# Optimization experiments

Hardware: AMD Instinct MI355X
Metric: run time of the kernel (lower is better)

The kernel has to match this reference:

```python
import jax, jax.numpy as jnp
import numpy as np

DIM = 1024
H = 16
HD = DIM // H  # 64
SCALE = HD ** -0.5
EPS = 1e-5


def setup_inputs() -> dict:
    key = jax.random.key(0)
    ks = jax.random.split(key, 8)
    B, N = 2, 2048
    x = jax.random.normal(ks[0], (B, N, DIM), dtype=jnp.float32)
    qkv_w = jax.random.normal(ks[1], (5 * DIM, DIM), dtype=jnp.float32) * (DIM ** -0.5)
    proj_w = jax.random.normal(ks[2], (DIM, DIM), dtype=jnp.float32) * (DIM ** -0.5)
    proj_b = jnp.zeros((DIM,), dtype=jnp.float32)
    lambda_q1 = jax.random.normal(ks[3], (HD,), dtype=jnp.float32) * 0.1
    lambda_k1 = jax.random.normal(ks[4], (HD,), dtype=jnp.float32) * 0.1
    lambda_q2 = jax.random.normal(ks[5], (HD,), dtype=jnp.float32) * 0.1
    lambda_k2 = jax.random.normal(ks[6], (HD,), dtype=jnp.float32) * 0.1
    return {"x": x, "qkv_w": qkv_w, "proj_w": proj_w, "proj_b": proj_b,
            "lambda_q1": lambda_q1, "lambda_k1": lambda_k1,
            "lambda_q2": lambda_q2, "lambda_k2": lambda_k2}


def reference(x, qkv_w, proj_w, proj_b, lambda_q1, lambda_k1, lambda_q2, lambda_k2):
    B, N, C = x.shape
    # qkv projection -> (5, B, H, N, hd)
    qkv = jnp.einsum('bnc,fc->bnf', x, qkv_w).reshape(B, N, 5, H, HD)
    qkv = jnp.transpose(qkv, (2, 0, 3, 1, 4))
    q1, q2, k1, k2, v = qkv[0], qkv[1], qkv[2], qkv[3], qkv[4]
    # dual attention score matrices (B, H, N, N)
    attn1 = jax.nn.softmax(jnp.einsum('bhqd,bhkd->bhqk', q1, k1) * SCALE, axis=-1)
    attn2 = jax.nn.softmax(jnp.einsum('bhqd,bhkd->bhqk', q2, k2) * SCALE, axis=-1)
    lambda_full = (jnp.exp(jnp.sum(lambda_q1 * lambda_k1))
                   - jnp.exp(jnp.sum(lambda_q2 * lambda_k2)) + 0.8)
    attn = attn1 - lambda_full * attn2
    out = jnp.einsum('bhqk,bhkd->bhqd', attn, v)  # (B,H,N,hd)
    out = jnp.transpose(out, (0, 2, 1, 3)).reshape(B, N, C)
    # RMSNorm (no affine) over last dim, then fixed scale (1 - 0.8)
    out = out * jax.lax.rsqrt(jnp.mean(out * out, axis=-1, keepdims=True) + EPS)
    out = out * (1.0 - 0.8)
    return jnp.einsum('bnc,oc->bno', out, proj_w) + proj_b
```

## Files before the change

### kernel.cpp

```cpp
#include <hip/hip_runtime.h>
#include <hip/hip_bf16.h>

#define SEQ   2048
#define BATCH 2
#define NHEAD 16
#define HDIM  64
#define CDIM  1024
#define QKV_F 5120
#define SCALE 0.125f
#define LOG2E 1.44269504f
#define EPSV  1e-5f

typedef __bf16 bf16;
typedef __bf16 bf16x4 __attribute__((ext_vector_type(4)));
typedef __bf16 bf16x8 __attribute__((ext_vector_type(8)));
typedef float  f32x4  __attribute__((ext_vector_type(4)));

#define MFMA16(a, b, c) __builtin_amdgcn_mfma_f32_16x16x32_bf16(a, b, c, 0, 0, 0)

__device__ __forceinline__ unsigned pkbf(float a, float b) {
    union { bf16 h[2]; unsigned u; } t;
    t.h[0] = (bf16)a; t.h[1] = (bf16)b;
    return t.u;
}
__device__ __forceinline__ unsigned short bfbits(float a) {
    union { bf16 h; unsigned short u; } t;
    t.h = (bf16)a;
    return t.u;
}
__device__ __forceinline__ void gload16(const void* g, void* l) {
    __builtin_amdgcn_global_load_lds(
        (const __attribute__((address_space(1))) unsigned int*)g,
        (__attribute__((address_space(3))) unsigned int*)l, 16, 0, 0);
}

__global__ __launch_bounds__(256) void cvt_bf16(
    const float* __restrict__ s, bf16* __restrict__ d)
{
    const int i = (blockIdx.x * 256 + threadIdx.x) * 8;
    float4 a = *(const float4*)(s + i);
    float4 b = *(const float4*)(s + i + 4);
    bf16x8 t;
    t[0] = (bf16)a.x; t[1] = (bf16)a.y; t[2] = (bf16)a.z; t[3] = (bf16)a.w;
    t[4] = (bf16)b.x; t[5] = (bf16)b.y; t[6] = (bf16)b.z; t[7] = (bf16)b.w;
    *(bf16x8*)(d + i) = t;
}

template <int EPI>
__global__ __launch_bounds__(256) void gemm_lds(
    const bf16* __restrict__ A, const bf16* __restrict__ Bw,
    const float* __restrict__ bias,
    bf16* __restrict__ outq, float* __restrict__ outp,
    int M, int Nn, int K)
{
    __shared__ __align__(16) bf16 As[128 * 64];
    __shared__ __align__(16) bf16 Bs[128 * 64];

    const int tid  = threadIdx.x;
    const int lane = tid & 63;
    const int wave = tid >> 6;
    const int wr = wave >> 1, wc = wave & 1;
    const int g = lane >> 4, fr = lane & 15;
    const int m0 = blockIdx.y * 128;
    const int n0 = blockIdx.x * 128;

    const int lrow = lane >> 3;
    const int lcol = (lane & 7) << 3;

    f32x4 acc[4][4];
#pragma unroll
    for (int m = 0; m < 4; ++m)
#pragma unroll
        for (int n = 0; n < 4; ++n) acc[m][n] = f32x4{0.f, 0.f, 0.f, 0.f};

    const int nkt = K >> 6;
    for (int kt = 0; kt < nkt; ++kt) {
        const int k0 = kt << 6;
        __syncthreads();
#pragma unroll
        for (int i = 0; i < 4; ++i) {
            const int chunk = wave * 4 + i;
            const int row = chunk * 8 + lrow;
            gload16(A + (size_t)(m0 + row) * K + k0 + lcol, As + chunk * 512);
            gload16(Bw + (size_t)(n0 + row) * K + k0 + lcol, Bs + chunk * 512);
        }
        __syncthreads();
#pragma unroll
        for (int ks = 0; ks < 2; ++ks) {
            bf16x8 af[4], bfr[4];
#pragma unroll
            for (int m = 0; m < 4; ++m)
                af[m] = *(const bf16x8*)(As + (wr * 64 + m * 16 + fr) * 64 + ks * 32 + g * 8);
#pragma unroll
            for (int n = 0; n < 4; ++n)
                bfr[n] = *(const bf16x8*)(Bs + (wc * 64 + n * 16 + fr) * 64 + ks * 32 + g * 8);
#pragma unroll
            for (int m = 0; m < 4; ++m)
#pragma unroll
                for (int n = 0; n < 4; ++n)
                    acc[m][n] = MFMA16(af[m], bfr[n], acc[m][n]);
        }
    }

#pragma unroll
    for (int m = 0; m < 4; ++m) {
#pragma unroll
        for (int n = 0; n < 4; ++n) {
            const int row0 = m0 + wr * 64 + m * 16 + g * 4;
            const int col  = n0 + wc * 64 + n * 16 + fr;
            if (EPI == 0) {
                const int bb = row0 >> 11, nn = row0 & (SEQ - 1);
                const int sI = col >> 10, rem = col & (CDIM - 1);
                const int hh = rem >> 6, dd = rem & 63;
                const size_t base = ((size_t)((sI * BATCH + bb) * NHEAD + hh)) << 17;
                if (sI == 4) {
                    const int t4 = (nn >> 2) & 15;
                    const int G = t4 >> 3, jh = (t4 >> 2) & 1, gg = t4 & 3;
                    const int u = (G << 3) | (gg << 1) | jh;
                    const int nnp = (nn & ~63) | (u << 2);
                    ushort4 uu;
                    uu.x = bfbits(acc[m][n][0]);
                    uu.y = bfbits(acc[m][n][1]);
                    uu.z = bfbits(acc[m][n][2]);
                    uu.w = bfbits(acc[m][n][3]);
                    *(ushort4*)(outq + base + ((size_t)dd << 11) + nnp) = uu;
                } else {
                    const float sc = (sI < 2) ? SCALE * LOG2E : 1.f;
#pragma unroll
                    for (int r = 0; r < 4; ++r)
                        outq[base + ((size_t)(nn + r) << 6) + dd] = (bf16)(acc[m][n][r] * sc);
                }
            } else {
#pragma unroll
                for (int r = 0; r < 4; ++r)
                    outp[(size_t)(row0 + r) * Nn + col] = acc[m][n][r] + bias[col];
            }
        }
    }
}

__global__ __launch_bounds__(512, 2) void diff_attn(
    const bf16* __restrict__ qkv,
    const float* __restrict__ lq1, const float* __restrict__ lk1,
    const float* __restrict__ lq2, const float* __restrict__ lk2,
    float* __restrict__ attn_out)
{
    __shared__ __align__(16) char SM[49152];

    const int tid = threadIdx.x;
    const int lane = tid & 63, wave = tid >> 6;
    const int wg = wave & 3, grp = wave >> 2;
    const int g = lane >> 4, fr = lane & 15;
    const int bh = blockIdx.x, b = bh >> 4, h = bh & 15;
    const int q0 = blockIdx.y * 64 + wg * 16;
    const int kv0 = grp * (SEQ / 2);

    float ls1 = 0.f, ls2 = 0.f;
    for (int i = 0; i < HDIM; ++i) { ls1 += lq1[i] * lk1[i]; ls2 += lq2[i] * lk2[i]; }
    const float lam = __expf(ls1) - __expf(ls2) + 0.8f;

    const size_t HS = (size_t)SEQ * HDIM;
    const char* q1p = (const char*)(qkv + ((size_t)((0 * BATCH + b) * NHEAD + h)) * HS);
    const char* q2p = (const char*)(qkv + ((size_t)((1 * BATCH + b) * NHEAD + h)) * HS);
    const char* k1p = (const char*)(qkv + ((size_t)((2 * BATCH + b) * NHEAD + h)) * HS);
    const char* k2p = (const char*)(qkv + ((size_t)((3 * BATCH + b) * NHEAD + h)) * HS);
    const char* vtp = (const char*)(qkv + ((size_t)((4 * BATCH + b) * NHEAD + h)) * HS);

    bf16x8 qf1[2], qf2[2];
#pragma unroll
    for (int ks = 0; ks < 2; ++ks) {
        qf1[ks] = *(const bf16x8*)(q1p + (size_t)(q0 + fr) * 128 + ks * 64 + g * 16);
        qf2[ks] = *(const bf16x8*)(q2p + (size_t)(q0 + fr) * 128 + ks * 64 + g * 16);
    }

    const f32x4 z4{0.f, 0.f, 0.f, 0.f};
    f32x4 o1[4], o2[4];
#pragma unroll
    for (int d = 0; d < 4; ++d) { o1[d] = z4; o2[d] = z4; }
    f32x4 l1v = z4, l2v = z4;
    float m1 = -1e30f, m2 = -1e30f;

    const int lrow8 = lane >> 3;
    const int scol  = ((lane & 7) ^ lrow8) << 4;
    const int xw    = (fr & 7) << 4;

    char* base = SM + grp * 24576;
    const char* K1s = base;
    const char* K2s = base + 8192;
    const char* Vts = base + 16384;

    auto smax = [&](f32x4& s0, f32x4& s1, f32x4& s2, f32x4& s3,
                    float& mS, f32x4& lv, f32x4* o, unsigned* pw) {
        f32x4 t = __builtin_elementwise_max(
            __builtin_elementwise_max(s0, s1), __builtin_elementwise_max(s2, s3));
        float pm = fmaxf(fmaxf(t[0], t[1]), fmaxf(t[2], t[3]));
        pm = fmaxf(pm, __shfl_xor(pm, 16));
        pm = fmaxf(pm, __shfl_xor(pm, 32));
        if (!__all(pm <= mS + 8.f * LOG2E)) {
            float mn = fmaxf(mS, pm);
            float alpha = __builtin_amdgcn_exp2f(mS - mn);
            lv *= alpha;
#pragma unroll
            for (int d = 0; d < 4; ++d) o[d] *= alpha;
            mS = mn;
        }
#pragma unroll
        for (int r = 0; r < 4; ++r) {
            s0[r] = __builtin_amdgcn_exp2f(s0[r] - mS);
            s1[r] = __builtin_amdgcn_exp2f(s1[r] - mS);
            s2[r] = __builtin_amdgcn_exp2f(s2[r] - mS);
            s3[r] = __builtin_amdgcn_exp2f(s3[r] - mS);
        }
        lv += (s0 + s1) + (s2 + s3);
        pw[0] = pkbf(s0[0], s0[1]); pw[1] = pkbf(s0[2], s0[3]);
        pw[2] = pkbf(s1[0], s1[1]); pw[3] = pkbf(s1[2], s1[3]);
        pw[4] = pkbf(s2[0], s2[1]); pw[5] = pkbf(s2[2], s2[3]);
        pw[6] = pkbf(s3[0], s3[1]); pw[7] = pkbf(s3[2], s3[3]);
    };

#define KRD(Ks, n, ks) (*(const bf16x8*)((Ks) + ((n) * 16 + fr) * 128 + (((ks) * 64 + g * 16) ^ xw)))

    for (int kt = 0; kt < SEQ / 2 / 64; ++kt) {
        const int kvb = kv0 + kt * 64;
        __syncthreads();
#pragma unroll
        for (int i = 0; i < 6; ++i) {
            const int c = wg * 6 + i;
            const int t = c >> 3, ch = c & 7;
            const int row = ch * 8 + lrow8;
            char* ldst = base + t * 8192 + ch * 1024;
            const char* src;
            if (t == 0)      src = k1p + (size_t)(kvb + row) * 128 + scol;
            else if (t == 1) src = k2p + (size_t)(kvb + row) * 128 + scol;
            else             src = vtp + (size_t)row * (SEQ * 2) + (size_t)kvb * 2 + scol;
            gload16(src, ldst);
        }
        __syncthreads();

        f32x4 s10, s11, s12, s13;
        __builtin_amdgcn_s_setprio(1);
        s10 = MFMA16(KRD(K1s, 0, 0), qf1[0], z4);
        s11 = MFMA16(KRD(K1s, 1, 0), qf1[0], z4);
        s12 = MFMA16(KRD(K1s, 2, 0), qf1[0], z4);
        s13 = MFMA16(KRD(K1s, 3, 0), qf1[0], z4);
        s10 = MFMA16(KRD(K1s, 0, 1), qf1[1], s10);
        s11 = MFMA16(KRD(K1s, 1, 1), qf1[1], s11);
        s12 = MFMA16(KRD(K1s, 2, 1), qf1[1], s12);
        s13 = MFMA16(KRD(K1s, 3, 1), qf1[1], s13);
        __builtin_amdgcn_s_setprio(0);
        unsigned p1w[8];
        smax(s10, s11, s12, s13, m1, l1v, o1, p1w);

        f32x4 s20, s21, s22, s23;
        __builtin_amdgcn_s_setprio(1);
        s20 = MFMA16(KRD(K2s, 0, 0), qf2[0], z4);
        s21 = MFMA16(KRD(K2s, 1, 0), qf2[0], z4);
        s22 = MFMA16(KRD(K2s, 2, 0), qf2[0], z4);
        s23 = MFMA16(KRD(K2s, 3, 0), qf2[0], z4);
        s20 = MFMA16(KRD(K2s, 0, 1), qf2[1], s20);
        s21 = MFMA16(KRD(K2s, 1, 1), qf2[1], s21);
        s22 = MFMA16(KRD(K2s, 2, 1), qf2[1], s22);
        s23 = MFMA16(KRD(K2s, 3, 1), qf2[1], s23);
        __builtin_amdgcn_s_setprio(0);
        unsigned p2w[8];
        smax(s20, s21, s22, s23, m2, l2v, o2, p2w);

        __builtin_amdgcn_s_setprio(1);
#pragma unroll
        for (int G = 0; G < 2; ++G) {
            union { unsigned u[4]; bf16x8 v; } pf1, pf2;
#pragma unroll
            for (int w = 0; w < 4; ++w) { pf1.u[w] = p1w[G * 4 + w]; pf2.u[w] = p2w[G * 4 + w]; }
#pragma unroll
            for (int ds = 0; ds < 4; ++ds) {
                const int vrow = ds * 16 + fr;
                bf16x8 vf = *(const bf16x8*)(Vts + vrow * 128 +
                              ((G * 64 + g * 16) ^ ((vrow & 7) << 4)));
                o1[ds] = MFMA16(vf, pf1.v, o1[ds]);
                o2[ds] = MFMA16(vf, pf2.v, o2[ds]);
            }
        }
        __builtin_amdgcn_s_setprio(0);
    }
#undef KRD

    float l1 = (l1v[0] + l1v[1]) + (l1v[2] + l1v[3]);
    float l2 = (l2v[0] + l2v[1]) + (l2v[2] + l2v[3]);
    l1 += __shfl_xor(l1, 16); l1 += __shfl_xor(l1, 32);
    l2 += __shfl_xor(l2, 16); l2 += __shfl_xor(l2, 32);

    float* MF = (float*)SM;
    float* OF = (float*)(SM + 4096);
    __syncthreads();
    if (grp == 1) {
        const int p = tid - 256;
        MF[0 * 256 + p] = m1; MF[1 * 256 + p] = l1;
        MF[2 * 256 + p] = m2; MF[3 * 256 + p] = l2;
#pragma unroll
        for (int ds = 0; ds < 4; ++ds)
#pragma unroll
            for (int r = 0; r < 4; ++r) {
                OF[(ds * 4 + r) * 256 + p]        = o1[ds][r];
                OF[(16 + ds * 4 + r) * 256 + p]   = o2[ds][r];
            }
    }
    __syncthreads();
    if (grp == 0) {
        const float mB1 = MF[0 * 256 + tid], lB1 = MF[1 * 256 + tid];
        const float mB2 = MF[2 * 256 + tid], lB2 = MF[3 * 256 + tid];
        const float mn1 = fmaxf(m1, mB1), mn2 = fmaxf(m2, mB2);
        const float aA1 = __builtin_amdgcn_exp2f(m1 - mn1);
        const float aB1 = __builtin_amdgcn_exp2f(mB1 - mn1);
        const float aA2 = __builtin_amdgcn_exp2f(m2 - mn2);
        const float aB2 = __builtin_amdgcn_exp2f(mB2 - mn2);
        const float L1 = l1 * aA1 + lB1 * aB1;
        const float L2 = l2 * aA2 + lB2 * aB2;
        const float i1 = 1.f / L1;
        const float i2 = lam / L2;
        float* op = attn_out + ((size_t)(b * SEQ + q0 + fr)) * CDIM + h * HDIM;
#pragma unroll
        for (int ds = 0; ds < 4; ++ds) {
            float4 o;
#pragma unroll
            for (int r = 0; r < 4; ++r) {
                const float v1 = o1[ds][r] * aA1 + OF[(ds * 4 + r) * 256 + tid] * aB1;
                const float v2 = o2[ds][r] * aA2 + OF[(16 + ds * 4 + r) * 256 + tid] * aB2;
                ((float*)&o)[r] = v1 * i1 - i2 * v2;
            }
            *(float4*)(op + ds * 16 + g * 4) = o;
        }
    }
}

__global__ __launch_bounds__(256) void rmsnorm_bf16(
    const float* __restrict__ in, bf16* __restrict__ out)
{
    __shared__ float red[4];
    const int row = blockIdx.x, tid = threadIdx.x;
    const float4 v = ((const float4*)(in + (size_t)row * CDIM))[tid];
    float ss = v.x * v.x + v.y * v.y + v.z * v.z + v.w * v.w;
#pragma unroll
    for (int m = 1; m < 64; m <<= 1) ss += __shfl_xor(ss, m);
    if ((tid & 63) == 0) red[tid >> 6] = ss;
    __syncthreads();
    float tot = red[0] + red[1] + red[2] + red[3];
    float sc = rsqrtf(tot * (1.f / CDIM) + EPSV) * 0.2f;
    bf16x4 o;
    o[0] = (bf16)(v.x * sc); o[1] = (bf16)(v.y * sc);
    o[2] = (bf16)(v.z * sc); o[3] = (bf16)(v.w * sc);
    ((bf16x4*)(out + (size_t)row * CDIM))[tid] = o;
}

extern "C" void kernel_launch(void* const* d_in, const int* in_sizes, int n_in,
                              void* d_out, int out_size, void* d_ws, size_t ws_size,
                              hipStream_t stream)
{
    (void)in_sizes; (void)n_in; (void)out_size; (void)ws_size;
    const float* x      = (const float*)d_in[0];
    const float* qkv_w  = (const float*)d_in[1];
    const float* proj_w = (const float*)d_in[2];
    const float* proj_b = (const float*)d_in[3];
    const float* lq1    = (const float*)d_in[4];
    const float* lk1    = (const float*)d_in[5];
    const float* lq2    = (const float*)d_in[6];
    const float* lk2    = (const float*)d_in[7];
    float* out = (float*)d_out;

    char* ws = (char*)d_ws;
    bf16*  qkv_t    = (bf16*)ws;
    bf16*  attn_b   = (bf16*)ws;
    float* attn_out = (float*)(ws + (size_t)40 * 1024 * 1024);
    bf16*  x_b      = (bf16*)(ws + (size_t)40 * 1024 * 1024);
    bf16*  qkvw_b   = (bf16*)(ws + (size_t)56 * 1024 * 1024);
    bf16*  projw_b  = (bf16*)(ws + (size_t)66 * 1024 * 1024);

    dim3 blk(256);
    cvt_bf16<<<dim3((BATCH * SEQ * CDIM) / 2048), blk, 0, stream>>>(x, x_b);
    cvt_bf16<<<dim3((QKV_F * CDIM) / 2048), blk, 0, stream>>>(qkv_w, qkvw_b);
    cvt_bf16<<<dim3((CDIM * CDIM) / 2048), blk, 0, stream>>>(proj_w, projw_b);
    gemm_lds<0><<<dim3(QKV_F / 128, (BATCH * SEQ) / 128), blk, 0, stream>>>(
        x_b, qkvw_b, nullptr, qkv_t, nullptr, BATCH * SEQ, QKV_F, CDIM);
    diff_attn<<<dim3(BATCH * NHEAD, SEQ / 64), dim3(512), 0, stream>>>(
        qkv_t, lq1, lk1, lq2, lk2, attn_out);
    rmsnorm_bf16<<<dim3(BATCH * SEQ), blk, 0, stream>>>(attn_out, attn_b);
    gemm_lds<1><<<dim3(CDIM / 128, (BATCH * SEQ) / 128), blk, 0, stream>>>(
        attn_b, projw_b, proj_b, nullptr, out, BATCH * SEQ, CDIM, CDIM);
}
```

Measured before the change: 273.8 us.

## Drop split-KV in diff attention, use 256-thread blocks, fuse conversions

The attention kernel no longer splits the KV range across two wave groups with an LDS merge. Each 256-thread block now walks all 2048 keys itself, which removes the cross-group reduction and its two barriers, halves LDS per block and raises the launch bound to 4 blocks per CU. In exchange each block runs a loop twice as long, with fewer waves to hide load latency. The three fp32-to-bf16 conversion launches are also merged into one kernel that picks its source by block index, saving two launches.

```diff
diff --git a/kernel.cpp b/kernel.cpp
--- a/kernel.cpp
+++ b/kernel.cpp
@@ -34,10 +34,19 @@
         (__attribute__((address_space(3))) unsigned int*)l, 16, 0, 0);
 }
 
-__global__ __launch_bounds__(256) void cvt_bf16(
-    const float* __restrict__ s, bf16* __restrict__ d)
-{
-    const int i = (blockIdx.x * 256 + threadIdx.x) * 8;
+__global__ __launch_bounds__(256) void cvt_all(
+    const float* __restrict__ x,  bf16* __restrict__ xb,
+    const float* __restrict__ qw, bf16* __restrict__ qwb,
+    const float* __restrict__ pw, bf16* __restrict__ pwb)
+{
+    const int bid = blockIdx.x;
+    const float* s;
+    bf16* d;
+    int off;
+    if (bid < 2048)      { s = x;  d = xb;  off = bid; }
+    else if (bid < 4608) { s = qw; d = qwb; off = bid - 2048; }
+    else                 { s = pw; d = pwb; off = bid - 4608; }
+    const int i = (off * 256 + threadIdx.x) * 8;
     float4 a = *(const float4*)(s + i);
     float4 b = *(const float4*)(s + i + 4);
     bf16x8 t;
@@ -139,21 +148,19 @@
     }
 }
 
-__global__ __launch_bounds__(512, 2) void diff_attn(
+__global__ __launch_bounds__(256, 4) void diff_attn(
     const bf16* __restrict__ qkv,
     const float* __restrict__ lq1, const float* __restrict__ lk1,
     const float* __restrict__ lq2, const float* __restrict__ lk2,
     float* __restrict__ attn_out)
 {
-    __shared__ __align__(16) char SM[49152];
+    __shared__ __align__(16) char SM[24576];
 
     const int tid = threadIdx.x;
     const int lane = tid & 63, wave = tid >> 6;
-    const int wg = wave & 3, grp = wave >> 2;
     const int g = lane >> 4, fr = lane & 15;
     const int bh = blockIdx.x, b = bh >> 4, h = bh & 15;
-    const int q0 = blockIdx.y * 64 + wg * 16;
-    const int kv0 = grp * (SEQ / 2);
+    const int q0 = blockIdx.y * 64 + wave * 16;
 
     float ls1 = 0.f, ls2 = 0.f;
     for (int i = 0; i < HDIM; ++i) { ls1 += lq1[i] * lk1[i]; ls2 += lq2[i] * lk2[i]; }
@@ -184,10 +191,9 @@
     const int scol  = ((lane & 7) ^ lrow8) << 4;
     const int xw    = (fr & 7) << 4;
 
-    char* base = SM + grp * 24576;
-    const char* K1s = base;
-    const char* K2s = base + 8192;
-    const char* Vts = base + 16384;
+    const char* K1s = SM;
+    const char* K2s = SM + 8192;
+    const char* Vts = SM + 16384;
 
     auto smax = [&](f32x4& s0, f32x4& s1, f32x4& s2, f32x4& s3,
                     float& mS, f32x4& lv, f32x4* o, unsigned* pw) {
@@ -220,15 +226,15 @@
 
 #define KRD(Ks, n, ks) (*(const bf16x8*)((Ks) + ((n) * 16 + fr) * 128 + (((ks) * 64 + g * 16) ^ xw)))
 
-    for (int kt = 0; kt < SEQ / 2 / 64; ++kt) {
-        const int kvb = kv0 + kt * 64;
+    for (int kt = 0; kt < SEQ / 64; ++kt) {
+        const int kvb = kt * 64;
         __syncthreads();
 #pragma unroll
         for (int i = 0; i < 6; ++i) {
-            const int c = wg * 6 + i;
+            const int c = wave * 6 + i;
             const int t = c >> 3, ch = c & 7;
             const int row = ch * 8 + lrow8;
-            char* ldst = base + t * 8192 + ch * 1024;
+            char* ldst = SM + t * 8192 + ch * 1024;
             const char* src;
             if (t == 0)      src = k1p + (size_t)(kvb + row) * 128 + scol;
             else if (t == 1) src = k2p + (size_t)(kvb + row) * 128 + scol;
@@ -289,46 +295,17 @@
     l1 += __shfl_xor(l1, 16); l1 += __shfl_xor(l1, 32);
     l2 += __shfl_xor(l2, 16); l2 += __shfl_xor(l2, 32);
 
-    float* MF = (float*)SM;
-    float* OF = (float*)(SM + 4096);
-    __syncthreads();
-    if (grp == 1) {
-        const int p = tid - 256;
-        MF[0 * 256 + p] = m1; MF[1 * 256 + p] = l1;
-        MF[2 * 256 + p] = m2; MF[3 * 256 + p] = l2;
-#pragma unroll
-        for (int ds = 0; ds < 4; ++ds)
-#pragma unroll
-            for (int r = 0; r < 4; ++r) {
-                OF[(ds * 4 + r) * 256 + p]        = o1[ds][r];
-                OF[(16 + ds * 4 + r) * 256 + p]   = o2[ds][r];
-            }
-    }
-    __syncthreads();
-    if (grp == 0) {
-        const float mB1 = MF[0 * 256 + tid], lB1 = MF[1 * 256 + tid];
-        const float mB2 = MF[2 * 256 + tid], lB2 = MF[3 * 256 + tid];
-        const float mn1 = fmaxf(m1, mB1), mn2 = fmaxf(m2, mB2);
-        const float aA1 = __builtin_amdgcn_exp2f(m1 - mn1);
-        const float aB1 = __builtin_amdgcn_exp2f(mB1 - mn1);
-        const float aA2 = __builtin_amdgcn_exp2f(m2 - mn2);
-        const float aB2 = __builtin_amdgcn_exp2f(mB2 - mn2);
-        const float L1 = l1 * aA1 + lB1 * aB1;
-        const float L2 = l2 * aA2 + lB2 * aB2;
-        const float i1 = 1.f / L1;
-        const float i2 = lam / L2;
-        float* op = attn_out + ((size_t)(b * SEQ + q0 + fr)) * CDIM + h * HDIM;
-#pragma unroll
-        for (int ds = 0; ds < 4; ++ds) {
-            float4 o;
-#pragma unroll
-            for (int r = 0; r < 4; ++r) {
-                const float v1 = o1[ds][r] * aA1 + OF[(ds * 4 + r) * 256 + tid] * aB1;
-                const float v2 = o2[ds][r] * aA2 + OF[(16 + ds * 4 + r) * 256 + tid] * aB2;
-                ((float*)&o)[r] = v1 * i1 - i2 * v2;
-            }
-            *(float4*)(op + ds * 16 + g * 4) = o;
-        }
+    const float i1 = 1.f / l1;
+    const float i2 = lam / l2;
+    float* op = attn_out + ((size_t)(b * SEQ + q0 + fr)) * CDIM + h * HDIM;
+#pragma unroll
+    for (int ds = 0; ds < 4; ++ds) {
+        float4 o;
+        o.x = o1[ds][0] * i1 - i2 * o2[ds][0];
+        o.y = o1[ds][1] * i1 - i2 * o2[ds][1];
+        o.z = o1[ds][2] * i1 - i2 * o2[ds][2];
+        o.w = o1[ds][3] * i1 - i2 * o2[ds][3];
+        *(float4*)(op + ds * 16 + g * 4) = o;
     }
 }
 
@@ -375,12 +352,10 @@
     bf16*  projw_b  = (bf16*)(ws + (size_t)66 * 1024 * 1024);
 
     dim3 blk(256);
-    cvt_bf16<<<dim3((BATCH * SEQ * CDIM) / 2048), blk, 0, stream>>>(x, x_b);
-    cvt_bf16<<<dim3((QKV_F * CDIM) / 2048), blk, 0, stream>>>(qkv_w, qkvw_b);
-    cvt_bf16<<<dim3((CDIM * CDIM) / 2048), blk, 0, stream>>>(proj_w, projw_b);
+    cvt_all<<<dim3(5120), blk, 0, stream>>>(x, x_b, qkv_w, qkvw_b, proj_w, projw_b);
     gemm_lds<0><<<dim3(QKV_F / 128, (BATCH * SEQ) / 128), blk, 0, stream>>>(
         x_b, qkvw_b, nullptr, qkv_t, nullptr, BATCH * SEQ, QKV_F, CDIM);
-    diff_attn<<<dim3(BATCH * NHEAD, SEQ / 64), dim3(512), 0, stream>>>(
+    diff_attn<<<dim3(BATCH * NHEAD, SEQ / 64), blk, 0, stream>>>(
         qkv_t, lq1, lk1, lq2, lk2, attn_out);
     rmsnorm_bf16<<<dim3(BATCH * SEQ), blk, 0, stream>>>(attn_out, attn_b);
     gemm_lds<1><<<dim3(CDIM / 128, (BATCH * SEQ) / 128), blk, 0, stream>>>(
```

Result: faster. 244.0 us (-10.9%).
